# Kernel optimization log

Measured on AMD Instinct MI355X. Metric: run time of the kernel, lower is better.

The kernel has to match this reference:

```python
import jax, jax.numpy as jnp
import numpy as np

STRIDE, PAD, DIL = 1, 1, 1
EPS = 1e-12
RHO_LIM = 1.0 - 1e-6
PI = jnp.pi


def clamp_pg(x, lo=0.0):
    # clamp value but pass gradient through (clamp_preserve_grad)
    return x + jax.lax.stop_gradient(jnp.maximum(x, lo) - x)


def setup_inputs() -> dict:
    key = jax.random.key(0)
    B, N, T, K = 8, 128, 1024, 3
    k = jax.random.uniform(key, (B, B, N, T, 2), dtype=jnp.float32)
    leak = jnp.array(1.0, dtype=jnp.float32)
    alpha = jnp.full((1, 1, K), 1.0 / K, dtype=jnp.float32)
    beta = jnp.array(0.0, dtype=jnp.float32)
    return {"k": k, "leak": leak, "alpha": alpha, "beta": beta}


def reference(k, leak, alpha, beta):
    k_gp, k_ntk = k[..., 0], k[..., 1]          # (B,B,N,T) each
    B, _, N, T = k_gp.shape

    # v[b,t] = k_gp[b,b,0,t]  (diagonal over batch dims, first lag)
    ar = jnp.arange(B)
    v = k_gp[ar, ar, 0, :]                      # (B,T)
    v_pad = jnp.pad(v, ((0, 0), (0, N - 1)))    # (B, T+N-1)

    v_xx = v[:, None, None, :]                  # (B,1,1,T)
    idx = jnp.arange(N)[:, None] + jnp.arange(T)[None, :]  # (N,T)
    v_yy = v_pad[:, idx][None]                  # (1,B,N,T): v_pad[b, n+t]

    # calculate_statistics
    std_x = jnp.sqrt(jnp.maximum(v_xx, 0.0))
    std_y = jnp.sqrt(jnp.maximum(v_yy, 0.0))
    denom = jnp.maximum(std_x * std_y, EPS)
    rho = jnp.clip(k_gp / denom, -RHO_LIM, RHO_LIM)  # (B,B,N,T)

    a = clamp_pg(leak)
    theta = jnp.arccos(rho)
    s = jnp.sqrt(1.0 - rho * rho)
    one_m = (1.0 - a) ** 2
    coef = 1.0 + a * a
    # leaky-ReLU arccos kernel and its derivative kernel
    c0 = std_x * std_y / (2.0 * PI) * (one_m * s + rho * (coef * PI - one_m * theta))
    c1 = (coef * PI - one_m * theta) / (2.0 * PI)

    w = clamp_pg(alpha)                         # (1,1,K)

    def conv(x):  # x: (B,B,N,T) -> (B,B,N,T')
        y = jax.lax.conv_general_dilated(
            x.reshape(-1, 1, T), w, window_strides=(STRIDE,),
            padding=[(PAD, PAD)], rhs_dilation=(DIL,),
            dimension_numbers=("NCH", "OIH", "NCH"))
        return y.reshape(B, B, N, -1)

    kg = conv(c0)
    kn = conv(c1 * k_ntk) + kg

    b = clamp_pg(beta)
    kg = kg + b
    kn = kn + b
    return jnp.stack([kg, kn], axis=-1)
```

## Files before the change

kernel.cpp:

```cpp
#include <hip/hip_runtime.h>
#include <math.h>

#define BDIM 8
#define NDIM 128
#define TDIM 1024
#define TPB 512
#define CT 64
#define RPI 16
#define NIT (NDIM / RPI)
#define SXN (CT + 2)
#define SYN (NDIM + CT + 1)

#define EPS_F 1e-12f
#define RHO_LIM_F (1.0f - 1e-6f)
#define PI_F 3.14159265358979323846f

typedef float nfloat4 __attribute__((ext_vector_type(4)));

__device__ __forceinline__ void kfun(float kgp, float kntk, float sx, float sy,
                                     float one_m, float coef, bool fast,
                                     float& c0, float& cn)
{
    const float inv2pi = 0.15915494309189535f;
    const float p = sx * sy;
    if (fast) {
        const float hc = 0.5f * coef;
        const float pr = p * RHO_LIM_F;
        c0 = hc * fminf(fmaxf(kgp, -pr), pr);
        cn = hc * kntk;
    } else {
        const float r  = fminf(fmaxf(kgp * __builtin_amdgcn_rcpf(fmaxf(p, EPS_F)), -RHO_LIM_F), RHO_LIM_F);
        const float th = acosf(r);
        const float s  = sqrtf(1.0f - r * r);
        const float br = coef * PI_F - one_m * th;
        c0 = p * inv2pi * (one_m * s + r * br);
        cn = br * inv2pi * kntk;
    }
}

__global__ __launch_bounds__(TPB) void conv_arccos_kernel(
    const float* __restrict__ k,
    const float* __restrict__ leak,
    const float* __restrict__ alpha,
    const float* __restrict__ beta,
    float* __restrict__ out)
{
    __shared__ float sx_lds[SXN];
    __shared__ float sy_lds[SYN];

    const int chunk = blockIdx.x & 15;
    const int bb    = blockIdx.x >> 4;
    const int b2    = bb & (BDIM - 1);
    const int b1    = bb >> 3;
    const int tc    = chunk * CT;

    const int tid  = threadIdx.x;
    const int r_t  = tid & 31;
    const int rsel = tid >> 5;

    const float a   = fmaxf(leak[0], 0.0f);
    const float w0  = fmaxf(alpha[0], 0.0f);
    const float w1  = fmaxf(alpha[1], 0.0f);
    const float w2  = fmaxf(alpha[2], 0.0f);
    const float bia = fmaxf(beta[0], 0.0f);

    const float one_m = (1.0f - a) * (1.0f - a);
    const float coef  = 1.0f + a * a;
    const bool  fast  = (one_m == 0.0f);

    const float2* vrx = (const float2*)k + (size_t)(b1 * BDIM + b1) * NDIM * TDIM;
    const float2* vry = (const float2*)k + (size_t)(b2 * BDIM + b2) * NDIM * TDIM;

    if (tid < SXN) {
        const int t = tc - 1 + tid;
        const float v = (t >= 0 && t < TDIM) ? vrx[t].x : 0.0f;
        sx_lds[tid] = sqrtf(fmaxf(v, 0.0f));
    } else if (tid < SXN + SYN) {
        const int j = tid - SXN;
        const int e = tc - 1 + j;
        const float v = (e >= 0 && e < TDIM) ? vry[e].x : 0.0f;
        sy_lds[j] = sqrtf(fmaxf(v, 0.0f));
    }
    __syncthreads();

    const float sxm = sx_lds[2 * r_t];
    const float sx0 = sx_lds[2 * r_t + 1];
    const float sx1 = sx_lds[2 * r_t + 2];
    const float sxp = sx_lds[2 * r_t + 3];

    const int  t0     = tc + 2 * r_t;
    const bool lvalid = (t0 > 0);
    const bool rvalid = (t0 + 2 < TDIM);
    const int  eli    = max(t0 - 1, 0);
    const int  eri    = min(t0 + 2, TDIM - 1);
    const int  f      = (tc >> 1) + r_t;

    #pragma unroll 2
    for (int i = 0; i < NIT; ++i) {
        const int n   = i * RPI + rsel;
        const int row = bb * NDIM + n;
        const float*  krow  = k + (size_t)row * (TDIM * 2);
        const float2* krow2 = (const float2*)krow;

        const nfloat4 kv = *((const nfloat4*)krow + f);
        const float2  kl = krow2[eli];
        const float2  kr = krow2[eri];
        const float klg = lvalid ? kl.x : 0.0f;
        const float kln = lvalid ? kl.y : 0.0f;
        const float krg = rvalid ? kr.x : 0.0f;
        const float krn = rvalid ? kr.y : 0.0f;

        const int jy = n + 2 * r_t + 1;
        const float sym = sy_lds[jy - 1];
        const float sy0 = sy_lds[jy];
        const float sy1 = sy_lds[jy + 1];
        const float syp = sy_lds[jy + 2];

        float c0l, cnl, c00, cn0, c01, cn1, c0r, cnr;
        kfun(klg,  kln,  sxm, sym, one_m, coef, fast, c0l, cnl);
        kfun(kv.x, kv.y, sx0, sy0, one_m, coef, fast, c00, cn0);
        kfun(kv.z, kv.w, sx1, sy1, one_m, coef, fast, c01, cn1);
        kfun(krg,  krn,  sxp, syp, one_m, coef, fast, c0r, cnr);

        const float kg0 = fmaf(w0, c0l, fmaf(w1, c00, fmaf(w2, c01, bia)));
        const float kg1 = fmaf(w0, c00, fmaf(w1, c01, fmaf(w2, c0r, bia)));
        const float kn0 = fmaf(w0, cnl, fmaf(w1, cn0, fmaf(w2, cn1, kg0)));
        const float kn1 = fmaf(w0, cn0, fmaf(w1, cn1, fmaf(w2, cnr, kg1)));

        nfloat4 o;
        o.x = kg0; o.y = kn0; o.z = kg1; o.w = kn1;
        __builtin_nontemporal_store(o, (nfloat4*)(out + (size_t)row * (TDIM * 2)) + f);
    }
}

extern "C" void kernel_launch(void* const* d_in, const int* in_sizes, int n_in,
                              void* d_out, int out_size, void* d_ws, size_t ws_size,
                              hipStream_t stream) {
    const float* k     = (const float*)d_in[0];
    const float* leak  = (const float*)d_in[1];
    const float* alpha = (const float*)d_in[2];
    const float* beta  = (const float*)d_in[3];
    float* out = (float*)d_out;

    const int n_blocks = BDIM * BDIM * (TDIM / CT);
    conv_arccos_kernel<<<n_blocks, TPB, 0, stream>>>(k, leak, alpha, beta, out);
}
```

Measured before the change: 120.8 us.

## Use wavefront-wide rows with shuffle-based halo exchange instead of redundant neighbor loads

```diff
diff --git a/kernel.cpp b/kernel.cpp
--- a/kernel.cpp
+++ b/kernel.cpp
@@ -4,18 +4,17 @@
 #define BDIM 8
 #define NDIM 128
 #define TDIM 1024
-#define TPB 512
-#define CT 64
-#define RPI 16
-#define NIT (NDIM / RPI)
+#define TPB 1024
+#define CT 128
+#define NCHUNK (TDIM / CT)
+#define WPB (TPB / 64)
+#define NIT (NDIM / WPB)
 #define SXN (CT + 2)
 #define SYN (NDIM + CT + 1)
 
 #define EPS_F 1e-12f
 #define RHO_LIM_F (1.0f - 1e-6f)
 #define PI_F 3.14159265358979323846f
-
-typedef float nfloat4 __attribute__((ext_vector_type(4)));
 
 __device__ __forceinline__ void kfun(float kgp, float kntk, float sx, float sy,
                                      float one_m, float coef, bool fast,
@@ -48,15 +47,15 @@
     __shared__ float sx_lds[SXN];
     __shared__ float sy_lds[SYN];
 
-    const int chunk = blockIdx.x & 15;
-    const int bb    = blockIdx.x >> 4;
+    const int chunk = blockIdx.x & (NCHUNK - 1);
+    const int bb    = blockIdx.x >> 3;
     const int b2    = bb & (BDIM - 1);
     const int b1    = bb >> 3;
     const int tc    = chunk * CT;
 
     const int tid  = threadIdx.x;
-    const int r_t  = tid & 31;
-    const int rsel = tid >> 5;
+    const int lane = tid & 63;
+    const int wid  = tid >> 6;
 
     const float a   = fmaxf(leak[0], 0.0f);
     const float w0  = fmaxf(alpha[0], 0.0f);
@@ -83,53 +82,52 @@
     }
     __syncthreads();
 
-    const float sxm = sx_lds[2 * r_t];
-    const float sx0 = sx_lds[2 * r_t + 1];
-    const float sx1 = sx_lds[2 * r_t + 2];
-    const float sxp = sx_lds[2 * r_t + 3];
+    const float sx0 = sx_lds[2 * lane + 1];
+    const float sx1 = sx_lds[2 * lane + 2];
+    const float sxm = sx_lds[0];
+    const float sxp = sx_lds[CT + 1];
 
-    const int  t0     = tc + 2 * r_t;
-    const bool lvalid = (t0 > 0);
-    const bool rvalid = (t0 + 2 < TDIM);
-    const int  eli    = max(t0 - 1, 0);
-    const int  eri    = min(t0 + 2, TDIM - 1);
-    const int  f      = (tc >> 1) + r_t;
+    const bool lhalo = (lane == 0)  && (tc > 0);
+    const bool rhalo = (lane == 63) && (tc + CT < TDIM);
+    const int  g     = (tc >> 1) + lane;
 
     #pragma unroll 2
     for (int i = 0; i < NIT; ++i) {
-        const int n   = i * RPI + rsel;
+        const int n   = i * WPB + wid;
         const int row = bb * NDIM + n;
-        const float*  krow  = k + (size_t)row * (TDIM * 2);
-        const float2* krow2 = (const float2*)krow;
+        const float* krow = k + (size_t)row * (TDIM * 2);
 
-        const nfloat4 kv = *((const nfloat4*)krow + f);
-        const float2  kl = krow2[eli];
-        const float2  kr = krow2[eri];
-        const float klg = lvalid ? kl.x : 0.0f;
-        const float kln = lvalid ? kl.y : 0.0f;
-        const float krg = rvalid ? kr.x : 0.0f;
-        const float krn = rvalid ? kr.y : 0.0f;
+        const float4 kv = ((const float4*)krow)[g];
+        const float sy0 = sy_lds[n + 2 * lane + 1];
+        const float sy1 = sy_lds[n + 2 * lane + 2];
 
-        const int jy = n + 2 * r_t + 1;
-        const float sym = sy_lds[jy - 1];
-        const float sy0 = sy_lds[jy];
-        const float sy1 = sy_lds[jy + 1];
-        const float syp = sy_lds[jy + 2];
-
-        float c0l, cnl, c00, cn0, c01, cn1, c0r, cnr;
-        kfun(klg,  kln,  sxm, sym, one_m, coef, fast, c0l, cnl);
+        float c00, cn0, c01, cn1;
         kfun(kv.x, kv.y, sx0, sy0, one_m, coef, fast, c00, cn0);
         kfun(kv.z, kv.w, sx1, sy1, one_m, coef, fast, c01, cn1);
-        kfun(krg,  krn,  sxp, syp, one_m, coef, fast, c0r, cnr);
+
+        float c0lh = 0.0f, cnlh = 0.0f, c0rh = 0.0f, cnrh = 0.0f;
+        if (lhalo) {
+            const float2 kl = ((const float2*)krow)[tc - 1];
+            kfun(kl.x, kl.y, sxm, sy_lds[n], one_m, coef, fast, c0lh, cnlh);
+        }
+        if (rhalo) {
+            const float2 kr = ((const float2*)krow)[tc + CT];
+            kfun(kr.x, kr.y, sxp, sy_lds[n + CT + 1], one_m, coef, fast, c0rh, cnrh);
+        }
+
+        float c0l = __shfl_up(c01, 1);
+        float cnl = __shfl_up(cn1, 1);
+        float c0r = __shfl_down(c00, 1);
+        float cnr = __shfl_down(cn0, 1);
+        if (lane == 0)  { c0l = c0lh; cnl = cnlh; }
+        if (lane == 63) { c0r = c0rh; cnr = cnrh; }
 
         const float kg0 = fmaf(w0, c0l, fmaf(w1, c00, fmaf(w2, c01, bia)));
         const float kg1 = fmaf(w0, c00, fmaf(w1, c01, fmaf(w2, c0r, bia)));
         const float kn0 = fmaf(w0, cnl, fmaf(w1, cn0, fmaf(w2, cn1, kg0)));
         const float kn1 = fmaf(w0, cn0, fmaf(w1, cn1, fmaf(w2, cnr, kg1)));
 
-        nfloat4 o;
-        o.x = kg0; o.y = kn0; o.z = kg1; o.w = kn1;
-        __builtin_nontemporal_store(o, (nfloat4*)(out + (size_t)row * (TDIM * 2)) + f);
+        ((float4*)(out + (size_t)row * (TDIM * 2)))[g] = make_float4(kg0, kn0, kg1, kn1);
     }
 }
 
@@ -142,6 +140,6 @@
     const float* beta  = (const float*)d_in[3];
     float* out = (float*)d_out;
 
-    const int n_blocks = BDIM * BDIM * (TDIM / CT);
+    const int n_blocks = BDIM * BDIM * NCHUNK;
     conv_arccos_kernel<<<n_blocks, TPB, 0, stream>>>(k, leak, alpha, beta, out);
 }
```

After: 122.1 us. No clear change (+1.1%).
